# Optimization experiments

Measured on AMD Instinct MI355X. Metric: run time of the kernel, lower is better.

## Reference

```python
import jax, jax.numpy as jnp
import numpy as np

B, S_DIM, A_DIM = 8192, 39, 4
D_IN = S_DIM + A_DIM  # 43
F = 1024              # n_features width
E = 8                 # n_experts
C = 10                # n_contexts
N_OUT = 1


def setup_inputs() -> dict:
    key = jax.random.key(0)
    ks = jax.random.split(key, 12)
    inp = {
        "state": jax.random.normal(ks[0], (B, S_DIM), jnp.float32),
        "action": jax.random.normal(ks[1], (B, A_DIM), jnp.float32),
        "c": jax.random.randint(ks[2], (B,), 0, C, jnp.int32),
        # per-expert backbone params (InputLayer+ParallelLayer => E independent MLPs)
        "W0": jax.random.normal(ks[3], (E, D_IN, F), jnp.float32) * 0.05,
        "b0": jnp.zeros((E, F), jnp.float32),
        "W1": jax.random.normal(ks[4], (E, F, F), jnp.float32) * 0.03,
        "b1": jnp.zeros((E, F), jnp.float32),
        # task encoder: Linear(n_contexts -> n_experts, bias=False), weight [E, C]
        "Wte": jax.random.normal(ks[5], (E, C), jnp.float32) * 0.3,
        # per-context output heads: Linear(F -> 1)
        "Wh": jax.random.normal(ks[6], (C, F, N_OUT), jnp.float32) * 0.03,
        "bh": jnp.zeros((C, N_OUT), jnp.float32),
    }
    return inp


def reference(state, action, c, W0, b0, W1, b1, Wte, Wh, bh):
    # mixture weights: one_hot(c) @ Wte^T  ==  Wte[:, c]^T  -> [B, E]
    w = Wte.T[c]                                            # [B, E]
    sa = jnp.concatenate([state, action], axis=1)           # [B, D_IN]
    # per-expert backbone MLP (ReLU after each layer, incl. last since activation='ReLU')
    h = jax.nn.relu(jnp.einsum('bi,eio->ebo', sa, W0) + b0[:, None, :])   # [E, B, F]
    h = jax.nn.relu(jnp.einsum('ebi,eio->ebo', h, W1) + b1[:, None, :])   # [E, B, F]
    feats = jnp.transpose(h, (1, 0, 2))                     # [B, E, F]
    feats = jax.nn.relu(feats)                              # agg_activation[0]
    mixed = jnp.einsum('be,bef->bf', w, feats)              # [B, F]
    mixed = jax.nn.relu(mixed)                              # agg_activation[1]
    # context-routed heads: gather each sample's head params (same math as the
    # unique-context scatter loop in the original)
    q = jnp.einsum('bf,bfo->bo', mixed, Wh[c]) + bh[c]      # [B, 1]
    return jnp.squeeze(q, axis=-1)                          # [B]
```

## Files before the change

kernel.cpp:

```cpp
#include <hip/hip_runtime.h>
#include <hip/hip_bf16.h>
#include <stdint.h>

typedef __attribute__((ext_vector_type(8))) __bf16 bf16x8;
typedef __attribute__((ext_vector_type(4))) float f32x4;

__device__ __forceinline__ unsigned short f2b(float f) {
    return __builtin_bit_cast(unsigned short, __float2bfloat16(f));
}

__device__ __forceinline__ void gload_lds16(const void* g, void* l) {
    __builtin_amdgcn_global_load_lds(
        (__attribute__((address_space(1))) void*)(uintptr_t)g,
        (__attribute__((address_space(3))) void*)l,
        16, 0, 0);
}

#define MFMA16(a, b, c) __builtin_amdgcn_mfma_f32_16x16x32_bf16((a), (b), (c), 0, 0, 0)


__global__ void k_prep_sa(const float* __restrict__ state, const float* __restrict__ action,
                          const int* __restrict__ c, const float* __restrict__ Wte,
                          unsigned short* __restrict__ SA, float* __restrict__ wmix, int B) {
    int b = blockIdx.x * 256 + threadIdx.x;
    if (b >= B) return;
    unsigned short* row = SA + (size_t)b * 64;
#pragma unroll
    for (int i = 0; i < 39; ++i) row[i] = f2b(state[(size_t)b * 39 + i]);
#pragma unroll
    for (int i = 0; i < 4; ++i) row[39 + i] = f2b(action[(size_t)b * 4 + i]);
#pragma unroll
    for (int i = 43; i < 64; ++i) row[i] = 0;
    int ctx = c[b];
#pragma unroll
    for (int e = 0; e < 8; ++e) wmix[(size_t)b * 8 + e] = Wte[e * 10 + ctx];
}

__global__ void k_prep_w0t(const float* __restrict__ W0, unsigned short* __restrict__ W0T) {
    int idx = blockIdx.x * 256 + threadIdx.x;
    int e = idx >> 10, f = idx & 1023;
    unsigned short* dst = W0T + (size_t)idx * 64;
#pragma unroll 1
    for (int k = 0; k < 43; ++k) dst[k] = f2b(W0[((size_t)e * 43 + k) * 1024 + f]);
#pragma unroll
    for (int k = 43; k < 64; ++k) dst[k] = 0;
}

__global__ void k_prep_w1t(const float* __restrict__ W1, unsigned short* __restrict__ W1T) {
    __shared__ float t[64][65];
    int k0 = blockIdx.x * 64, n0 = blockIdx.y * 64, e = blockIdx.z;
    int tid = threadIdx.x;
    int cl = tid & 63;
    int rg = tid >> 6;
    const float* src = W1 + ((size_t)e * 1024 + k0) * 1024 + n0;
#pragma unroll
    for (int i = 0; i < 16; ++i) {
        int kr = rg * 16 + i;
        t[kr][cl] = src[(size_t)kr * 1024 + cl];
    }
    __syncthreads();
    int nl = tid >> 2, kg = tid & 3;
    unsigned short* dst = W1T + ((size_t)e * 1024 + n0 + nl) * 1024 + k0 + kg * 16;
#pragma unroll
    for (int j = 0; j < 16; ++j) dst[j] = f2b(t[kg * 16 + j][nl]);
}

__global__ __launch_bounds__(256, 2)
void k_layer0(const unsigned short* __restrict__ SA,
              const unsigned short* __restrict__ W0T,
              const float* __restrict__ b0,
              unsigned short* __restrict__ H0,
              int Bc, int row0) {
    __shared__ unsigned short As[128 * 64];
    __shared__ unsigned short Bs[128 * 64];
    int bm = blockIdx.x, bn = blockIdx.y, e = blockIdx.z;
    int tid = threadIdx.x, lane = tid & 63;
    int wv = tid >> 6, wr = wv >> 1, wc = wv & 1;
    int l15 = lane & 15, kg = lane >> 4;

    const char* Ag = (const char*)(SA + (size_t)(row0 + bm * 128) * 64);
    const char* Bg = (const char*)(W0T + ((size_t)e * 1024 + bn * 128) * 64);
#pragma unroll
    for (int it = 0; it < 4; ++it) {
        int off = tid * 16 + it * 4096;
        gload_lds16(Ag + off, (char*)As + off);
        gload_lds16(Bg + off, (char*)Bs + off);
    }
    __syncthreads();

    f32x4 acc[4][4];
#pragma unroll
    for (int mi = 0; mi < 4; ++mi)
#pragma unroll
        for (int ni = 0; ni < 4; ++ni) acc[mi][ni] = (f32x4)0.0f;

#pragma unroll
    for (int ks = 0; ks < 2; ++ks) {
        bf16x8 af[4], bv[4];
#pragma unroll
        for (int mi = 0; mi < 4; ++mi)
            af[mi] = *(const bf16x8*)&As[(wr * 64 + mi * 16 + l15) * 64 + ks * 32 + kg * 8];
#pragma unroll
        for (int ni = 0; ni < 4; ++ni)
            bv[ni] = *(const bf16x8*)&Bs[(wc * 64 + ni * 16 + l15) * 64 + ks * 32 + kg * 8];
#pragma unroll
        for (int mi = 0; mi < 4; ++mi)
#pragma unroll
            for (int ni = 0; ni < 4; ++ni)
                acc[mi][ni] = MFMA16(af[mi], bv[ni], acc[mi][ni]);
    }

    float b0v[4];
#pragma unroll
    for (int ni = 0; ni < 4; ++ni)
        b0v[ni] = b0[e * 1024 + bn * 128 + wc * 64 + ni * 16 + l15];
#pragma unroll
    for (int mi = 0; mi < 4; ++mi)
#pragma unroll
        for (int ni = 0; ni < 4; ++ni)
#pragma unroll
            for (int j = 0; j < 4; ++j) {
                int rloc = bm * 128 + wr * 64 + mi * 16 + kg * 4 + j;
                int col = bn * 128 + wc * 64 + ni * 16 + l15;
                float h = fmaxf(acc[mi][ni][j] + b0v[ni], 0.0f);
                H0[((size_t)e * Bc + rloc) * 1024 + col] = f2b(h);
            }
}

__global__ __launch_bounds__(256, 2)
void k_layer1_mix(const unsigned short* __restrict__ H0,
                  const unsigned short* __restrict__ W1T,
                  const float* __restrict__ b1,
                  const float* __restrict__ wmix,
                  float* __restrict__ mixed,
                  int Bc, int row0) {
    __shared__ unsigned short As[2][128 * 64];
    __shared__ unsigned short Bs[2][128 * 64];
    __shared__ float wmixLds[128 * 8];
    __shared__ float b1Lds[8 * 128];

    int nbm = Bc / 128;
    int wg = blockIdx.x;
    int bm, bn;
    if ((nbm & 7) == 0) {
        int xcd = wg & 7, j = wg >> 3;
        bm = xcd + ((j >> 3) << 3);
        bn = j & 7;
    } else {
        bm = wg >> 3;
        bn = wg & 7;
    }

    int tid = threadIdx.x, lane = tid & 63;
    int wv = tid >> 6;
    int wr = wv >> 1, wc = wv & 1;
    int l15 = lane & 15, kg = lane >> 4;
    int kg16 = kg * 16;
    int xsw = (l15 & 7) << 4;

    int tid16 = tid * 16;
    int sSrc[4], sDst[4];
#pragma unroll
    for (int i = 0; i < 4; ++i) {
        int flat = tid16 + i * 4096;
        int row = flat >> 7, colb = flat & 127;
        sDst[i] = flat;
        sSrc[i] = row * 2048 + (colb ^ ((row & 7) << 4));
    }

    const char* h0base = (const char*)H0 + (size_t)(bm * 128) * 2048;
    const char* w1base = (const char*)W1T + (size_t)(bn * 128) * 2048;
    size_t eAstride = (size_t)Bc * 2048;

    int aOff[4], bOff[4];
#pragma unroll
    for (int m = 0; m < 4; ++m) aOff[m] = (wr * 64 + m * 16 + l15) * 128;
#pragma unroll
    for (int n = 0; n < 4; ++n) bOff[n] = (wc * 64 + n * 16 + l15) * 128;

    for (int idx = tid; idx < 1024; idx += 256) {
        int r = idx >> 3, e = idx & 7;
        wmixLds[idx] = wmix[(size_t)(row0 + bm * 128 + r) * 8 + e];
    }
    for (int idx = tid; idx < 1024; idx += 256)
        b1Lds[idx] = b1[(idx >> 7) * 1024 + bn * 128 + (idx & 127)];
    __syncthreads();

    f32x4 acc[4][4], mix[4][4];
#pragma unroll
    for (int m = 0; m < 4; ++m)
#pragma unroll
        for (int n = 0; n < 4; ++n) { acc[m][n] = (f32x4)0.0f; mix[m][n] = (f32x4)0.0f; }

    const int NT = 128;

    auto STAGE_PA = [&](int tt) {
        int e = tt >> 4;
        int k0b = (tt & 15) << 7;
        const char* Ab = h0base + (size_t)e * eAstride + k0b;
        const char* Bb = w1base + (size_t)e * (1024 * 2048) + k0b;
        char* Ad = (char*)As[tt & 1];
        char* Bd = (char*)Bs[tt & 1];
        gload_lds16(Bb + sSrc[0], Bd + sDst[0]);
        gload_lds16(Bb + sSrc[1], Bd + sDst[1]);
        gload_lds16(Bb + sSrc[2], Bd + sDst[2]);
        gload_lds16(Bb + sSrc[3], Bd + sDst[3]);
        gload_lds16(Ab + sSrc[0], Ad + sDst[0]);
        gload_lds16(Ab + sSrc[2], Ad + sDst[2]);
    };
    auto STAGE_PB = [&](int tt) {
        int e = tt >> 4;
        int k0b = (tt & 15) << 7;
        const char* Ab = h0base + (size_t)e * eAstride + k0b;
        char* Ad = (char*)As[tt & 1];
        gload_lds16(Ab + sSrc[1], Ad + sDst[1]);
        gload_lds16(Ab + sSrc[3], Ad + sDst[3]);
    };

#define KB0 ((kg16) ^ xsw)
#define KB1 ((64 + kg16) ^ xsw)

    STAGE_PA(0);
    STAGE_PB(0);
    asm volatile("s_waitcnt vmcnt(2)\n\ts_barrier" ::: "memory");

#pragma unroll 1
    for (int t = 0; t < NT; ++t) {
        const char* Ab = (const char*)As[t & 1];
        const char* Bb = (const char*)Bs[t & 1];

        bf16x8 bfr[4][2];
#pragma unroll
        for (int n = 0; n < 4; ++n) {
            bfr[n][0] = *(const bf16x8*)(Bb + bOff[n] + KB0);
            bfr[n][1] = *(const bf16x8*)(Bb + bOff[n] + KB1);
        }
        bf16x8 af[2][2];
#pragma unroll
        for (int m = 0; m < 2; ++m) {
            af[m][0] = *(const bf16x8*)(Ab + aOff[m] + KB0);
            af[m][1] = *(const bf16x8*)(Ab + aOff[m] + KB1);
        }
        if (t + 1 < NT) STAGE_PA(t + 1);
        asm volatile("s_barrier" ::: "memory");
        asm volatile("s_waitcnt lgkmcnt(0)" ::: "memory");
        __builtin_amdgcn_sched_barrier(0);
        __builtin_amdgcn_s_setprio(1);
#pragma unroll
        for (int k = 0; k < 2; ++k)
#pragma unroll
            for (int m = 0; m < 2; ++m)
#pragma unroll
                for (int n = 0; n < 4; ++n)
                    acc[m][n] = MFMA16(af[m][k], bfr[n][k], acc[m][n]);
        __builtin_amdgcn_s_setprio(0);
        __builtin_amdgcn_sched_barrier(0);
        if (t + 1 < NT)
            asm volatile("s_waitcnt vmcnt(6)\n\ts_barrier" ::: "memory");
        else
            asm volatile("s_waitcnt vmcnt(0)\n\ts_barrier" ::: "memory");

        bf16x8 ag[2][2];
#pragma unroll
        for (int m = 0; m < 2; ++m) {
            ag[m][0] = *(const bf16x8*)(Ab + aOff[2 + m] + KB0);
            ag[m][1] = *(const bf16x8*)(Ab + aOff[2 + m] + KB1);
        }
        if (t + 1 < NT) STAGE_PB(t + 1);
        asm volatile("s_barrier" ::: "memory");
        asm volatile("s_waitcnt lgkmcnt(0)" ::: "memory");
        __builtin_amdgcn_sched_barrier(0);
        __builtin_amdgcn_s_setprio(1);
#pragma unroll
        for (int k = 0; k < 2; ++k)
#pragma unroll
            for (int m = 0; m < 2; ++m)
#pragma unroll
                for (int n = 0; n < 4; ++n)
                    acc[2 + m][n] = MFMA16(ag[m][k], bfr[n][k], acc[2 + m][n]);
        __builtin_amdgcn_s_setprio(0);
        __builtin_amdgcn_sched_barrier(0);
        if (t + 1 < NT)
            asm volatile("s_waitcnt vmcnt(2)\n\ts_barrier" ::: "memory");
        else
            asm volatile("s_waitcnt vmcnt(0)\n\ts_barrier" ::: "memory");

        if ((t & 15) == 15) {
            int e = t >> 4;
            float b1v[4];
#pragma unroll
            for (int n = 0; n < 4; ++n)
                b1v[n] = b1Lds[e * 128 + wc * 64 + n * 16 + l15];
#pragma unroll
            for (int m = 0; m < 4; ++m)
#pragma unroll
                for (int j = 0; j < 4; ++j) {
                    int lrow = wr * 64 + m * 16 + kg * 4 + j;
                    float w = wmixLds[lrow * 8 + e];
#pragma unroll
                    for (int n = 0; n < 4; ++n) {
                        float h = fmaxf(acc[m][n][j] + b1v[n], 0.0f);
                        mix[m][n][j] += w * h;
                        acc[m][n][j] = 0.0f;
                    }
                }
        }
    }
#undef KB0
#undef KB1

#pragma unroll
    for (int m = 0; m < 4; ++m)
#pragma unroll
        for (int n = 0; n < 4; ++n)
#pragma unroll
            for (int j = 0; j < 4; ++j) {
                int lrow = wr * 64 + m * 16 + kg * 4 + j;
                int col = bn * 128 + wc * 64 + n * 16 + l15;
                mixed[(size_t)(bm * 128 + lrow) * 1024 + col] = fmaxf(mix[m][n][j], 0.0f);
            }
}

__global__ void k_head(const float* __restrict__ mixed, const float* __restrict__ Wh,
                       const float* __restrict__ bh, const int* __restrict__ c,
                       float* __restrict__ q, int Bc, int row0) {
    int row = blockIdx.x * 4 + (threadIdx.x >> 6);
    int lane = threadIdx.x & 63;
    if (row >= Bc) return;
    int grow = row0 + row;
    int ctx = c[grow];
    const float4* m4 = (const float4*)(mixed + (size_t)row * 1024);
    const float4* w4 = (const float4*)(Wh + (size_t)ctx * 1024);
    float s = 0.0f;
#pragma unroll
    for (int i = 0; i < 4; ++i) {
        float4 a = m4[lane + i * 64];
        float4 b = w4[lane + i * 64];
        s += a.x * b.x + a.y * b.y + a.z * b.z + a.w * b.w;
    }
#pragma unroll
    for (int off = 32; off > 0; off >>= 1) s += __shfl_down(s, off);
    if (lane == 0) q[grow] = s + bh[ctx];
}

extern "C" void kernel_launch(void* const* d_in, const int* in_sizes, int n_in,
                              void* d_out, int out_size, void* d_ws, size_t ws_size,
                              hipStream_t stream) {
    const float* state  = (const float*)d_in[0];
    const float* action = (const float*)d_in[1];
    const int*   c      = (const int*)d_in[2];
    const float* W0     = (const float*)d_in[3];
    const float* b0     = (const float*)d_in[4];
    const float* W1     = (const float*)d_in[5];
    const float* b1     = (const float*)d_in[6];
    const float* Wte    = (const float*)d_in[7];
    const float* Wh     = (const float*)d_in[8];
    const float* bh     = (const float*)d_in[9];
    float* q = (float*)d_out;
    int B = in_sizes[2];

    char* p = (char*)d_ws;
    unsigned short* W1T = (unsigned short*)p; p += (size_t)8 * 1024 * 1024 * 2;
    unsigned short* W0T = (unsigned short*)p; p += (size_t)8 * 1024 * 64 * 2;
    unsigned short* SA  = (unsigned short*)p; p += (size_t)B * 64 * 2;
    float* wmix         = (float*)p;          p += (size_t)B * 8 * 4;
    size_t fixed = (size_t)(p - (char*)d_ws);

    int Bc = B;
    while (Bc > 256 && fixed + (size_t)Bc * (8 * 1024 * 2 + 1024 * 4) > ws_size) Bc >>= 1;

    unsigned short* H0 = (unsigned short*)p; p += (size_t)8 * Bc * 1024 * 2;
    float* mixed       = (float*)p;

    k_prep_sa<<<(B + 255) / 256, 256, 0, stream>>>(state, action, c, Wte, SA, wmix, B);
    k_prep_w0t<<<(8 * 1024) / 256, 256, 0, stream>>>(W0, W0T);
    k_prep_w1t<<<dim3(16, 16, 8), 256, 0, stream>>>(W1, W1T);

    for (int row0 = 0; row0 < B; row0 += Bc) {
        k_layer0<<<dim3(Bc / 128, 8, 8), 256, 0, stream>>>(SA, W0T, b0, H0, Bc, row0);
        k_layer1_mix<<<(Bc / 128) * 8, 256, 0, stream>>>(H0, W1T, b1, wmix, mixed, Bc, row0);
        k_head<<<(Bc + 3) / 4, 256, 0, stream>>>(mixed, Wh, bh, c, q, Bc, row0);
    }
}
```

Before: 197.3 us.

## Fuse context head into layer-1 mix kernel via atomic partial dot products

The per-context output head is folded into the layer-1 GEMM epilogue. Each wave computes a partial dot product of its ReLU'd mixed tile with the gathered head weights, reduces across 16 lanes with shuffles, and atomically adds into q, which is zeroed by a memset first. This removes the fp32 mixed intermediate (B x 1024 write and reread) and the separate head launch. It also drops the workspace-size batch chunking and always processes the full batch in one pass, which assumes the workspace is large enough. In exchange it adds atomics, a memset, and nondeterministic summation order.

```diff
diff --git a/kernel.cpp b/kernel.cpp
--- a/kernel.cpp
+++ b/kernel.cpp
@@ -50,8 +50,7 @@
     __shared__ float t[64][65];
     int k0 = blockIdx.x * 64, n0 = blockIdx.y * 64, e = blockIdx.z;
     int tid = threadIdx.x;
-    int cl = tid & 63;
-    int rg = tid >> 6;
+    int cl = tid & 63, rg = tid >> 6;
     const float* src = W1 + ((size_t)e * 1024 + k0) * 1024 + n0;
 #pragma unroll
     for (int i = 0; i < 16; ++i) {
@@ -70,7 +69,7 @@
               const unsigned short* __restrict__ W0T,
               const float* __restrict__ b0,
               unsigned short* __restrict__ H0,
-              int Bc, int row0) {
+              int Btot) {
     __shared__ unsigned short As[128 * 64];
     __shared__ unsigned short Bs[128 * 64];
     int bm = blockIdx.x, bn = blockIdx.y, e = blockIdx.z;
@@ -78,7 +77,7 @@
     int wv = tid >> 6, wr = wv >> 1, wc = wv & 1;
     int l15 = lane & 15, kg = lane >> 4;
 
-    const char* Ag = (const char*)(SA + (size_t)(row0 + bm * 128) * 64);
+    const char* Ag = (const char*)(SA + (size_t)(bm * 128) * 64);
     const char* Bg = (const char*)(W0T + ((size_t)e * 1024 + bn * 128) * 64);
 #pragma unroll
     for (int it = 0; it < 4; ++it) {
@@ -123,23 +122,26 @@
                 int rloc = bm * 128 + wr * 64 + mi * 16 + kg * 4 + j;
                 int col = bn * 128 + wc * 64 + ni * 16 + l15;
                 float h = fmaxf(acc[mi][ni][j] + b0v[ni], 0.0f);
-                H0[((size_t)e * Bc + rloc) * 1024 + col] = f2b(h);
+                H0[((size_t)e * Btot + rloc) * 1024 + col] = f2b(h);
             }
 }
 
 __global__ __launch_bounds__(256, 2)
-void k_layer1_mix(const unsigned short* __restrict__ H0,
-                  const unsigned short* __restrict__ W1T,
-                  const float* __restrict__ b1,
-                  const float* __restrict__ wmix,
-                  float* __restrict__ mixed,
-                  int Bc, int row0) {
+void k_fused(const unsigned short* __restrict__ H0,
+             const unsigned short* __restrict__ W1T,
+             const float* __restrict__ b1,
+             const float* __restrict__ wmix,
+             const float* __restrict__ Wh,
+             const float* __restrict__ bh,
+             const int* __restrict__ c,
+             float* __restrict__ q,
+             int Btot) {
     __shared__ unsigned short As[2][128 * 64];
     __shared__ unsigned short Bs[2][128 * 64];
     __shared__ float wmixLds[128 * 8];
     __shared__ float b1Lds[8 * 128];
 
-    int nbm = Bc / 128;
+    int nbm = Btot / 128;
     int wg = blockIdx.x;
     int bm, bn;
     if ((nbm & 7) == 0) {
@@ -147,8 +149,7 @@
         bm = xcd + ((j >> 3) << 3);
         bn = j & 7;
     } else {
-        bm = wg >> 3;
-        bn = wg & 7;
+        bm = wg >> 3; bn = wg & 7;
     }
 
     int tid = threadIdx.x, lane = tid & 63;
@@ -170,7 +171,7 @@
 
     const char* h0base = (const char*)H0 + (size_t)(bm * 128) * 2048;
     const char* w1base = (const char*)W1T + (size_t)(bn * 128) * 2048;
-    size_t eAstride = (size_t)Bc * 2048;
+    size_t eAstride = (size_t)Btot * 2048;
 
     int aOff[4], bOff[4];
 #pragma unroll
@@ -180,7 +181,7 @@
 
     for (int idx = tid; idx < 1024; idx += 256) {
         int r = idx >> 3, e = idx & 7;
-        wmixLds[idx] = wmix[(size_t)(row0 + bm * 128 + r) * 8 + e];
+        wmixLds[idx] = wmix[(size_t)(bm * 128 + r) * 8 + e];
     }
     for (int idx = tid; idx < 1024; idx += 256)
         b1Lds[idx] = b1[(idx >> 7) * 1024 + bn * 128 + (idx & 127)];
@@ -312,35 +313,23 @@
 #pragma unroll
     for (int m = 0; m < 4; ++m)
 #pragma unroll
-        for (int n = 0; n < 4; ++n)
-#pragma unroll
-            for (int j = 0; j < 4; ++j) {
-                int lrow = wr * 64 + m * 16 + kg * 4 + j;
-                int col = bn * 128 + wc * 64 + n * 16 + l15;
-                mixed[(size_t)(bm * 128 + lrow) * 1024 + col] = fmaxf(mix[m][n][j], 0.0f);
+        for (int j = 0; j < 4; ++j) {
+            int grow = bm * 128 + wr * 64 + m * 16 + kg * 4 + j;
+            int ctx = c[grow];
+            const float* whp = Wh + (size_t)ctx * 1024 + bn * 128 + wc * 64;
+            float s = 0.0f;
+#pragma unroll
+            for (int n = 0; n < 4; ++n)
+                s += fmaxf(mix[m][n][j], 0.0f) * whp[n * 16 + l15];
+            s += __shfl_xor(s, 1);
+            s += __shfl_xor(s, 2);
+            s += __shfl_xor(s, 4);
+            s += __shfl_xor(s, 8);
+            if (l15 == 0) {
+                if (bn == 0 && wc == 0) s += bh[ctx];
+                atomicAdd(q + grow, s);
             }
-}
-
-__global__ void k_head(const float* __restrict__ mixed, const float* __restrict__ Wh,
-                       const float* __restrict__ bh, const int* __restrict__ c,
-                       float* __restrict__ q, int Bc, int row0) {
-    int row = blockIdx.x * 4 + (threadIdx.x >> 6);
-    int lane = threadIdx.x & 63;
-    if (row >= Bc) return;
-    int grow = row0 + row;
-    int ctx = c[grow];
-    const float4* m4 = (const float4*)(mixed + (size_t)row * 1024);
-    const float4* w4 = (const float4*)(Wh + (size_t)ctx * 1024);
-    float s = 0.0f;
-#pragma unroll
-    for (int i = 0; i < 4; ++i) {
-        float4 a = m4[lane + i * 64];
-        float4 b = w4[lane + i * 64];
-        s += a.x * b.x + a.y * b.y + a.z * b.z + a.w * b.w;
-    }
-#pragma unroll
-    for (int off = 32; off > 0; off >>= 1) s += __shfl_down(s, off);
-    if (lane == 0) q[grow] = s + bh[ctx];
+        }
 }
 
 extern "C" void kernel_launch(void* const* d_in, const int* in_sizes, int n_in,
@@ -364,21 +353,13 @@
     unsigned short* W0T = (unsigned short*)p; p += (size_t)8 * 1024 * 64 * 2;
     unsigned short* SA  = (unsigned short*)p; p += (size_t)B * 64 * 2;
     float* wmix         = (float*)p;          p += (size_t)B * 8 * 4;
-    size_t fixed = (size_t)(p - (char*)d_ws);
-
-    int Bc = B;
-    while (Bc > 256 && fixed + (size_t)Bc * (8 * 1024 * 2 + 1024 * 4) > ws_size) Bc >>= 1;
-
-    unsigned short* H0 = (unsigned short*)p; p += (size_t)8 * Bc * 1024 * 2;
-    float* mixed       = (float*)p;
+    unsigned short* H0  = (unsigned short*)p;
+
+    hipMemsetAsync(q, 0, (size_t)B * 4, stream);
 
     k_prep_sa<<<(B + 255) / 256, 256, 0, stream>>>(state, action, c, Wte, SA, wmix, B);
     k_prep_w0t<<<(8 * 1024) / 256, 256, 0, stream>>>(W0, W0T);
     k_prep_w1t<<<dim3(16, 16, 8), 256, 0, stream>>>(W1, W1T);
-
-    for (int row0 = 0; row0 < B; row0 += Bc) {
-        k_layer0<<<dim3(Bc / 128, 8, 8), 256, 0, stream>>>(SA, W0T, b0, H0, Bc, row0);
-        k_layer1_mix<<<(Bc / 128) * 8, 256, 0, stream>>>(H0, W1T, b1, wmix, mixed, Bc, row0);
-        k_head<<<(Bc + 3) / 4, 256, 0, stream>>>(mixed, Wh, bh, c, q, Bc, row0);
-    }
-}
+    k_layer0<<<dim3(B / 128, 8, 8), 256, 0, stream>>>(SA, W0T, b0, H0, B);
+    k_fused<<<(B / 128) * 8, 256, 0, stream>>>(H0, W1T, b1, wmix, Wh, bh, c, q, B);
+}
```

New measurement: 206.2 us. 1.04x slower.
